# Performance work log

Hardware: AMD Instinct MI355X
Metric: run time of the kernel (lower is better)

The kernel has to match this reference:

```python
import jax, jax.numpy as jnp
import numpy as np

N_NODES = 50000
N_EDGES = 800000
IN_FEATS = 512
NUM_HEADS = 4
OUT_FEATS = 64
NEG_SLOPE = 0.2


def setup_inputs() -> dict:
    key = jax.random.key(0)
    k1, k2, k3, k4, k5, k6 = jax.random.split(key, 6)
    feat = jax.random.normal(k1, (N_NODES, IN_FEATS), dtype=jnp.float32)
    W = jax.random.normal(k2, (IN_FEATS, NUM_HEADS * OUT_FEATS), dtype=jnp.float32) * (1.0 / np.sqrt(IN_FEATS))
    attn_l = jax.random.normal(k3, (NUM_HEADS, OUT_FEATS), dtype=jnp.float32) * (1.0 / np.sqrt(OUT_FEATS))
    attn_r = jax.random.normal(k4, (NUM_HEADS, OUT_FEATS), dtype=jnp.float32) * (1.0 / np.sqrt(OUT_FEATS))
    src = jax.random.randint(k5, (N_EDGES,), 0, N_NODES, dtype=jnp.int32)
    dst = jax.random.randint(k6, (N_EDGES,), 0, N_NODES, dtype=jnp.int32)
    return {"feat": feat, "W": W, "attn_l": attn_l, "attn_r": attn_r, "src": src, "dst": dst}


def reference(feat, W, attn_l, attn_r, src, dst):
    N = feat.shape[0]
    H, D = attn_l.shape
    # node-wise projection: fc(feat).view(N, H, D)
    ft = (feat @ W).reshape(N, H, D)
    # per-node attention logits
    el = jnp.einsum('nhd,hd->nh', ft, attn_l)  # [N, H]
    er = jnp.einsum('nhd,hd->nh', ft, attn_r)  # [N, H]
    # edge-wise score: leaky_relu(el[u] + er[v])
    e = jax.nn.leaky_relu(el[src] + er[dst], negative_slope=NEG_SLOPE)  # [E, H]
    # segment softmax over incoming edges of each destination node
    e_max = jax.ops.segment_max(e, dst, num_segments=N)  # [N, H]
    e_max = jnp.where(jnp.isfinite(e_max), e_max, 0.0)
    exp_e = jnp.exp(e - e_max[dst])  # [E, H]
    denom = jax.ops.segment_sum(exp_e, dst, num_segments=N)  # [N, H]
    a = exp_e / denom[dst]  # [E, H]
    # weighted message aggregation: sum_u a(u,v) * ft[u]
    msg = ft[src] * a[:, :, None]  # [E, H, D]
    out = jax.ops.segment_sum(msg, dst, num_segments=N)  # [N, H, D]
    return out.reshape(N, H * D)
```

## Files before the change

kernel.cpp:

```cpp
#include <hip/hip_runtime.h>
#include <hip/hip_fp16.h>

#define N_NODES 50000
#define N_EDGES 800000
#define IN_F    512
#define NH      4
#define DH      64
#define HD      256
#define NEG     0.2f
#define MAXDEG  64

typedef __attribute__((ext_vector_type(8))) short bf16x8;
typedef __attribute__((ext_vector_type(4))) float f32x4;

__device__ __forceinline__ unsigned short f2bf(float x) {
    unsigned u = __float_as_uint(x);
    unsigned r = (u + 0x7FFFu + ((u >> 16) & 1u)) >> 16;
    return (unsigned short)r;
}
__device__ __forceinline__ float bf2f(unsigned short b) {
    return __uint_as_float((unsigned)b << 16);
}
__device__ __forceinline__ unsigned short f2h(float x) {
    __half h = __float2half_rn(x);
    return *(unsigned short*)&h;
}
__device__ __forceinline__ float h2f(unsigned short us) {
    __half h = *(__half*)&us;
    return __half2float(h);
}

#define NZB ((N_NODES + 255) / 256)
__global__ __launch_bounds__(256) void setup_kernel(const float* __restrict__ W,
                                                    unsigned short* __restrict__ WtbT,
                                                    int* __restrict__ counts) {
    int b = blockIdx.x;
    if (b < NZB) {
        int i = b * 256 + threadIdx.x;
        if (i < N_NODES) counts[i] = 0;
    } else {
        int i = (b - NZB) * 256 + threadIdx.x;
        if (i < IN_F * HD) {
            int k = i >> 8;
            int n = i & 255;
            int t  = k >> 6;
            int kk = k & 63;
            int g  = kk >> 3;
            int w8 = kk & 7;
            int p  = n * 8 + (g ^ (n & 7));
            WtbT[(size_t)t * 16384 + p * 8 + w8] = f2bf(W[i]);
        }
    }
}

#define LDPA 72
__global__ __launch_bounds__(256) void gemm_kernel(const float* __restrict__ A,
                                                   const unsigned short* __restrict__ WtbT,
                                                   const float* __restrict__ attn_l,
                                                   const float* __restrict__ attn_r,
                                                   unsigned short* __restrict__ Cb,
                                                   float* __restrict__ el,
                                                   float* __restrict__ er) {
    __shared__ short A_s[64][LDPA];
    __shared__ short B_s[2][256 * 64];

    const int tid  = threadIdx.x;
    const int lane = tid & 63;
    const int w    = tid >> 6;
    const int lm   = lane & 15;
    const int quad = lane >> 4;
    const int row0 = blockIdx.x * 64;

    const int srow = tid >> 3;
    const int sc8  = (tid & 7) * 8;

    f32x4 acc[4][4] = {};
    float4 pa[4];

#define STAGE_B(BUF, T)                                                         \
    {                                                                           \
        const char* gsrc = (const char*)WtbT + (size_t)(T) * 32768 + tid * 16;  \
        char* ldst = (char*)&B_s[BUF][0] + tid * 16;                            \
        _Pragma("unroll")                                                       \
        for (int r = 0; r < 8; r++)                                             \
            __builtin_amdgcn_global_load_lds(                                   \
                (const __attribute__((address_space(1))) unsigned int*)(gsrc + r * 4096), \
                (__attribute__((address_space(3))) unsigned int*)(ldst + r * 4096),       \
                16, 0, 0);                                                      \
    }

#define LOAD_A(KT)                                                             \
    {                                                                          \
        int g0 = row0 + srow;                                                  \
        if (g0 < N_NODES) {                                                    \
            const float* ap = A + (size_t)g0 * IN_F + (KT) + sc8;              \
            pa[0] = *(const float4*)ap; pa[1] = *(const float4*)(ap + 4);      \
        } else { pa[0] = pa[1] = make_float4(0.f, 0.f, 0.f, 0.f); }            \
        int g1 = row0 + 32 + srow;                                             \
        if (g1 < N_NODES) {                                                    \
            const float* ap = A + (size_t)g1 * IN_F + (KT) + sc8;              \
            pa[2] = *(const float4*)ap; pa[3] = *(const float4*)(ap + 4);      \
        } else { pa[2] = pa[3] = make_float4(0.f, 0.f, 0.f, 0.f); }            \
    }

    STAGE_B(0, 0);
    LOAD_A(0);

    int buf = 0;
    for (int t = 0; t < 8; t++) {
        {
            bf16x8 s;
            s[0] = (short)f2bf(pa[0].x); s[1] = (short)f2bf(pa[0].y);
            s[2] = (short)f2bf(pa[0].z); s[3] = (short)f2bf(pa[0].w);
            s[4] = (short)f2bf(pa[1].x); s[5] = (short)f2bf(pa[1].y);
            s[6] = (short)f2bf(pa[1].z); s[7] = (short)f2bf(pa[1].w);
            *(bf16x8*)(&A_s[srow][sc8]) = s;
            s[0] = (short)f2bf(pa[2].x); s[1] = (short)f2bf(pa[2].y);
            s[2] = (short)f2bf(pa[2].z); s[3] = (short)f2bf(pa[2].w);
            s[4] = (short)f2bf(pa[3].x); s[5] = (short)f2bf(pa[3].y);
            s[6] = (short)f2bf(pa[3].z); s[7] = (short)f2bf(pa[3].w);
            *(bf16x8*)(&A_s[32 + srow][sc8]) = s;
        }
        __syncthreads();

        if (t + 1 < 8) { STAGE_B(buf ^ 1, t + 1); LOAD_A((t + 1) * 64); }

#pragma unroll
        for (int kk = 0; kk < 64; kk += 32) {
            bf16x8 af[4], bfr[4];
#pragma unroll
            for (int i = 0; i < 4; i++)
                af[i] = *(const bf16x8*)(&A_s[i * 16 + lm][kk + quad * 8]);
#pragma unroll
            for (int j = 0; j < 4; j++) {
                int n  = w * 64 + j * 16 + lm;
                int g  = (kk >> 3) + quad;
                int gs = g ^ (lm & 7);
                bfr[j] = *(const bf16x8*)(&B_s[buf][(n * 8 + gs) * 8]);
            }
#pragma unroll
            for (int i = 0; i < 4; i++)
#pragma unroll
                for (int j = 0; j < 4; j++)
                    acc[i][j] = __builtin_amdgcn_mfma_f32_16x16x32_bf16(
                        af[i], bfr[j], acc[i][j], 0, 0, 0);
        }
        if (t < 7) __syncthreads();
        buf ^= 1;
    }
#undef LOAD_A
#undef STAGE_B

#pragma unroll
    for (int i = 0; i < 4; i++) {
#pragma unroll
        for (int j = 0; j < 4; j++) {
            int gcol = w * 64 + j * 16 + lm;
#pragma unroll
            for (int r = 0; r < 4; r++) {
                int grow = row0 + i * 16 + quad * 4 + r;
                if (grow < N_NODES)
                    Cb[(size_t)grow * HD + gcol] = f2bf(acc[i][j][r]);
            }
        }
    }

    {
        float al[4], ar[4];
#pragma unroll
        for (int j = 0; j < 4; j++) {
            al[j] = attn_l[w * DH + j * 16 + lm];
            ar[j] = attn_r[w * DH + j * 16 + lm];
        }
#pragma unroll
        for (int i = 0; i < 4; i++) {
#pragma unroll
            for (int r = 0; r < 4; r++) {
                float sl = 0.f, sr = 0.f;
#pragma unroll
                for (int j = 0; j < 4; j++) {
                    sl += acc[i][j][r] * al[j];
                    sr += acc[i][j][r] * ar[j];
                }
#pragma unroll
                for (int off = 8; off > 0; off >>= 1) {
                    sl += __shfl_xor(sl, off);
                    sr += __shfl_xor(sr, off);
                }
                if (lm == 0) {
                    int grow = row0 + i * 16 + quad * 4 + r;
                    if (grow < N_NODES) {
                        el[(size_t)grow * NH + w] = sl;
                        er[(size_t)grow * NH + w] = sr;
                    }
                }
            }
        }
    }
}

__device__ __forceinline__ float lrelu_exp(float x) {
    float y = fmaxf(x, NEG * x);
    return fminf(__expf(y), 60000.f);
}

__global__ __launch_bounds__(256) void place_kernel(const int* __restrict__ src,
                                                    const int* __restrict__ dst,
                                                    const float* __restrict__ el,
                                                    const float* __restrict__ er,
                                                    int* __restrict__ counts,
                                                    int4* __restrict__ recs) {
    int e = blockIdx.x * blockDim.x + threadIdx.x;
    if (e >= N_EDGES) return;
    int u = src[e], v = dst[e];
    float4 l = *(const float4*)(el + (size_t)u * NH);
    float4 r = *(const float4*)(er + (size_t)v * NH);
    float w0 = lrelu_exp(l.x + r.x);
    float w1 = lrelu_exp(l.y + r.y);
    float w2 = lrelu_exp(l.z + r.z);
    float w3 = lrelu_exp(l.w + r.w);
    int4 rec;
    rec.x = u;
    rec.y = (int)(((unsigned)f2h(w1) << 16) | (unsigned)f2h(w0));
    rec.z = (int)(((unsigned)f2h(w3) << 16) | (unsigned)f2h(w2));
    rec.w = 0;
    int j = atomicAdd(&counts[v], 1);
    if (j < MAXDEG) recs[(size_t)v * MAXDEG + j] = rec;
}

__global__ __launch_bounds__(256) void agg_kernel(const unsigned short* __restrict__ ftb,
                                                  const int4* __restrict__ recs,
                                                  const int* __restrict__ counts,
                                                  float* __restrict__ out) {
    int wv   = (blockIdx.x * blockDim.x + threadIdx.x) >> 6;
    int lane = threadIdx.x & 63;
    if (wv >= N_NODES) return;

    int deg = counts[wv];
    deg = (deg > MAXDEG) ? MAXDEG : deg;
    const int h    = lane >> 4;
    const int sh   = (h & 1) * 16;
    const int wsel = 1 + (h >> 1);
    const size_t foff = (size_t)lane * 4;
    const unsigned* rp = (const unsigned*)(recs + (size_t)wv * MAXDEG);

    float4 acc = make_float4(0.f, 0.f, 0.f, 0.f);
    float dsum = 0.f;

    const int n8 = deg >> 3;
    for (int b = 0; b < n8; b++) {
        const unsigned* q = rp + b * 32;
        unsigned u0 = q[0],  p0 = q[0  + wsel];
        unsigned u1 = q[4],  p1 = q[4  + wsel];
        unsigned u2 = q[8],  p2 = q[8  + wsel];
        unsigned u3 = q[12], p3 = q[12 + wsel];
        unsigned u4 = q[16], p4 = q[16 + wsel];
        unsigned u5 = q[20], p5 = q[20 + wsel];
        unsigned u6 = q[24], p6 = q[24 + wsel];
        unsigned u7 = q[28], p7 = q[28 + wsel];
        ushort4 f0 = *(const ushort4*)(ftb + (size_t)u0 * HD + foff);
        ushort4 f1 = *(const ushort4*)(ftb + (size_t)u1 * HD + foff);
        ushort4 f2 = *(const ushort4*)(ftb + (size_t)u2 * HD + foff);
        ushort4 f3 = *(const ushort4*)(ftb + (size_t)u3 * HD + foff);
        ushort4 f4 = *(const ushort4*)(ftb + (size_t)u4 * HD + foff);
        ushort4 f5 = *(const ushort4*)(ftb + (size_t)u5 * HD + foff);
        ushort4 f6 = *(const ushort4*)(ftb + (size_t)u6 * HD + foff);
        ushort4 f7 = *(const ushort4*)(ftb + (size_t)u7 * HD + foff);
        float w0 = h2f((unsigned short)((p0 >> sh) & 0xFFFFu));
        float w1 = h2f((unsigned short)((p1 >> sh) & 0xFFFFu));
        float w2 = h2f((unsigned short)((p2 >> sh) & 0xFFFFu));
        float w3 = h2f((unsigned short)((p3 >> sh) & 0xFFFFu));
        float w4 = h2f((unsigned short)((p4 >> sh) & 0xFFFFu));
        float w5 = h2f((unsigned short)((p5 >> sh) & 0xFFFFu));
        float w6 = h2f((unsigned short)((p6 >> sh) & 0xFFFFu));
        float w7 = h2f((unsigned short)((p7 >> sh) & 0xFFFFu));
        acc.x += w0 * bf2f(f0.x) + w1 * bf2f(f1.x) + w2 * bf2f(f2.x) + w3 * bf2f(f3.x)
               + w4 * bf2f(f4.x) + w5 * bf2f(f5.x) + w6 * bf2f(f6.x) + w7 * bf2f(f7.x);
        acc.y += w0 * bf2f(f0.y) + w1 * bf2f(f1.y) + w2 * bf2f(f2.y) + w3 * bf2f(f3.y)
               + w4 * bf2f(f4.y) + w5 * bf2f(f5.y) + w6 * bf2f(f6.y) + w7 * bf2f(f7.y);
        acc.z += w0 * bf2f(f0.z) + w1 * bf2f(f1.z) + w2 * bf2f(f2.z) + w3 * bf2f(f3.z)
               + w4 * bf2f(f4.z) + w5 * bf2f(f5.z) + w6 * bf2f(f6.z) + w7 * bf2f(f7.z);
        acc.w += w0 * bf2f(f0.w) + w1 * bf2f(f1.w) + w2 * bf2f(f2.w) + w3 * bf2f(f3.w)
               + w4 * bf2f(f4.w) + w5 * bf2f(f5.w) + w6 * bf2f(f6.w) + w7 * bf2f(f7.w);
        dsum += ((w0 + w1) + (w2 + w3)) + ((w4 + w5) + (w6 + w7));
    }
    {
        const int p0i = n8 * 8;
        const int rem = deg - p0i;
        if (rem > 0) {
            const unsigned* q = rp + p0i * 4;
            unsigned u0 = q[0];
            unsigned u1 = (1 < rem) ? q[4]  : u0;
            unsigned u2 = (2 < rem) ? q[8]  : u0;
            unsigned u3 = (3 < rem) ? q[12] : u0;
            unsigned u4 = (4 < rem) ? q[16] : u0;
            unsigned u5 = (5 < rem) ? q[20] : u0;
            unsigned u6 = (6 < rem) ? q[24] : u0;
            unsigned p0 = q[0 + wsel];
            unsigned p1 = (1 < rem) ? q[4  + wsel] : 0u;
            unsigned p2 = (2 < rem) ? q[8  + wsel] : 0u;
            unsigned p3 = (3 < rem) ? q[12 + wsel] : 0u;
            unsigned p4 = (4 < rem) ? q[16 + wsel] : 0u;
            unsigned p5 = (5 < rem) ? q[20 + wsel] : 0u;
            unsigned p6 = (6 < rem) ? q[24 + wsel] : 0u;
            ushort4 f0 = *(const ushort4*)(ftb + (size_t)u0 * HD + foff);
            ushort4 f1 = *(const ushort4*)(ftb + (size_t)u1 * HD + foff);
            ushort4 f2 = *(const ushort4*)(ftb + (size_t)u2 * HD + foff);
            ushort4 f3 = *(const ushort4*)(ftb + (size_t)u3 * HD + foff);
            ushort4 f4 = *(const ushort4*)(ftb + (size_t)u4 * HD + foff);
            ushort4 f5 = *(const ushort4*)(ftb + (size_t)u5 * HD + foff);
            ushort4 f6 = *(const ushort4*)(ftb + (size_t)u6 * HD + foff);
            float w0 = h2f((unsigned short)((p0 >> sh) & 0xFFFFu));
            float w1 = h2f((unsigned short)((p1 >> sh) & 0xFFFFu));
            float w2 = h2f((unsigned short)((p2 >> sh) & 0xFFFFu));
            float w3 = h2f((unsigned short)((p3 >> sh) & 0xFFFFu));
            float w4 = h2f((unsigned short)((p4 >> sh) & 0xFFFFu));
            float w5 = h2f((unsigned short)((p5 >> sh) & 0xFFFFu));
            float w6 = h2f((unsigned short)((p6 >> sh) & 0xFFFFu));
            acc.x += w0 * bf2f(f0.x) + w1 * bf2f(f1.x) + w2 * bf2f(f2.x) + w3 * bf2f(f3.x)
                   + w4 * bf2f(f4.x) + w5 * bf2f(f5.x) + w6 * bf2f(f6.x);
            acc.y += w0 * bf2f(f0.y) + w1 * bf2f(f1.y) + w2 * bf2f(f2.y) + w3 * bf2f(f3.y)
                   + w4 * bf2f(f4.y) + w5 * bf2f(f5.y) + w6 * bf2f(f6.y);
            acc.z += w0 * bf2f(f0.z) + w1 * bf2f(f1.z) + w2 * bf2f(f2.z) + w3 * bf2f(f3.z)
                   + w4 * bf2f(f4.z) + w5 * bf2f(f5.z) + w6 * bf2f(f6.z);
            acc.w += w0 * bf2f(f0.w) + w1 * bf2f(f1.w) + w2 * bf2f(f2.w) + w3 * bf2f(f3.w)
                   + w4 * bf2f(f4.w) + w5 * bf2f(f5.w) + w6 * bf2f(f6.w);
            dsum += ((w0 + w1) + (w2 + w3)) + ((w4 + w5) + w6);
        }
    }

    float inv = (dsum > 0.f) ? (1.f / dsum) : 0.f;
    acc.x *= inv; acc.y *= inv; acc.z *= inv; acc.w *= inv;
    *(float4*)(out + (size_t)wv * HD + foff) = acc;
}

extern "C" void kernel_launch(void* const* d_in, const int* in_sizes, int n_in,
                              void* d_out, int out_size, void* d_ws, size_t ws_size,
                              hipStream_t stream) {
    const float* feat   = (const float*)d_in[0];
    const float* W      = (const float*)d_in[1];
    const float* attn_l = (const float*)d_in[2];
    const float* attn_r = (const float*)d_in[3];
    const int*   src    = (const int*)d_in[4];
    const int*   dst    = (const int*)d_in[5];
    float* out = (float*)d_out;

    char* p = (char*)d_ws;
    auto alloc = [&](size_t bytes) -> char* {
        char* r = p;
        p += (bytes + 255) & ~(size_t)255;
        return r;
    };
    unsigned short* ftb    = (unsigned short*)alloc((size_t)N_NODES * HD * 2);
    unsigned short* WtbT   = (unsigned short*)alloc((size_t)IN_F * HD * 2);
    float*          el     = (float*)alloc((size_t)N_NODES * NH * 4);
    float*          er     = (float*)alloc((size_t)N_NODES * NH * 4);
    int4*           recs   = (int4*)alloc((size_t)N_NODES * MAXDEG * 16);
    int*            counts = (int*)alloc((size_t)N_NODES * 4);

    setup_kernel<<<NZB + (IN_F * HD + 255) / 256, 256, 0, stream>>>(W, WtbT, counts);
    gemm_kernel<<<(N_NODES + 63) / 64, 256, 0, stream>>>(feat, WtbT, attn_l, attn_r,
                                                         ftb, el, er);
    place_kernel<<<(N_EDGES + 255) / 256, 256, 0, stream>>>(src, dst, el, er,
                                                            counts, recs);
    agg_kernel<<<(N_NODES + 3) / 4, 256, 0, stream>>>(ftb, recs, counts, out);
}
```

Measured before the change: 301.7 us.

## Load W fragments directly from global into registers; double-buffer A in LDS

The weight layout is changed to a k-group-major order so that each lane can read its B fragments for the MFMA straight from global memory (via L2) into registers. This removes the 64 KB B staging in LDS. The A tile is now double-buffered in LDS, which needs only one barrier per k-step instead of two, and row clamping replaces the branchy bounds checks. The cost is that every block issues redundant global reads of W, and global load latency now sits on the MFMA path. In exchange, LDS use drops sharply, which may allow higher occupancy.

```diff
diff --git a/kernel.cpp b/kernel.cpp
--- a/kernel.cpp
+++ b/kernel.cpp
@@ -47,8 +47,7 @@
             int kk = k & 63;
             int g  = kk >> 3;
             int w8 = kk & 7;
-            int p  = n * 8 + (g ^ (n & 7));
-            WtbT[(size_t)t * 16384 + p * 8 + w8] = f2bf(W[i]);
+            WtbT[(size_t)t * 16384 + g * 2048 + n * 8 + w8] = f2bf(W[i]);
         }
     }
 }
@@ -61,8 +60,7 @@
                                                    unsigned short* __restrict__ Cb,
                                                    float* __restrict__ el,
                                                    float* __restrict__ er) {
-    __shared__ short A_s[64][LDPA];
-    __shared__ short B_s[2][256 * 64];
+    __shared__ short A_s[2][64][LDPA];
 
     const int tid  = threadIdx.x;
     const int lane = tid & 63;
@@ -77,79 +75,79 @@
     f32x4 acc[4][4] = {};
     float4 pa[4];
 
-#define STAGE_B(BUF, T)                                                         \
-    {                                                                           \
-        const char* gsrc = (const char*)WtbT + (size_t)(T) * 32768 + tid * 16;  \
-        char* ldst = (char*)&B_s[BUF][0] + tid * 16;                            \
-        _Pragma("unroll")                                                       \
-        for (int r = 0; r < 8; r++)                                             \
-            __builtin_amdgcn_global_load_lds(                                   \
-                (const __attribute__((address_space(1))) unsigned int*)(gsrc + r * 4096), \
-                (__attribute__((address_space(3))) unsigned int*)(ldst + r * 4096),       \
-                16, 0, 0);                                                      \
-    }
-
 #define LOAD_A(KT)                                                             \
     {                                                                          \
-        int g0 = row0 + srow;                                                  \
-        if (g0 < N_NODES) {                                                    \
-            const float* ap = A + (size_t)g0 * IN_F + (KT) + sc8;              \
-            pa[0] = *(const float4*)ap; pa[1] = *(const float4*)(ap + 4);      \
-        } else { pa[0] = pa[1] = make_float4(0.f, 0.f, 0.f, 0.f); }            \
-        int g1 = row0 + 32 + srow;                                             \
-        if (g1 < N_NODES) {                                                    \
-            const float* ap = A + (size_t)g1 * IN_F + (KT) + sc8;              \
-            pa[2] = *(const float4*)ap; pa[3] = *(const float4*)(ap + 4);      \
-        } else { pa[2] = pa[3] = make_float4(0.f, 0.f, 0.f, 0.f); }            \
-    }
-
-    STAGE_B(0, 0);
+        int g0 = row0 + srow; g0 = (g0 < N_NODES) ? g0 : (N_NODES - 1);        \
+        const float* ap0 = A + (size_t)g0 * IN_F + (KT) + sc8;                 \
+        pa[0] = *(const float4*)ap0; pa[1] = *(const float4*)(ap0 + 4);        \
+        int g1 = row0 + 32 + srow; g1 = (g1 < N_NODES) ? g1 : (N_NODES - 1);   \
+        const float* ap1 = A + (size_t)g1 * IN_F + (KT) + sc8;                 \
+        pa[2] = *(const float4*)ap1; pa[3] = *(const float4*)(ap1 + 4);        \
+    }
+
+#define CVT_STORE(BUF)                                                         \
+    {                                                                          \
+        bf16x8 s;                                                              \
+        s[0] = (short)f2bf(pa[0].x); s[1] = (short)f2bf(pa[0].y);              \
+        s[2] = (short)f2bf(pa[0].z); s[3] = (short)f2bf(pa[0].w);              \
+        s[4] = (short)f2bf(pa[1].x); s[5] = (short)f2bf(pa[1].y);              \
+        s[6] = (short)f2bf(pa[1].z); s[7] = (short)f2bf(pa[1].w);              \
+        *(bf16x8*)(&A_s[BUF][srow][sc8]) = s;                                  \
+        s[0] = (short)f2bf(pa[2].x); s[1] = (short)f2bf(pa[2].y);              \
+        s[2] = (short)f2bf(pa[2].z); s[3] = (short)f2bf(pa[2].w);              \
+        s[4] = (short)f2bf(pa[3].x); s[5] = (short)f2bf(pa[3].y);              \
+        s[6] = (short)f2bf(pa[3].z); s[7] = (short)f2bf(pa[3].w);              \
+        *(bf16x8*)(&A_s[BUF][32 + srow][sc8]) = s;                             \
+    }
+
     LOAD_A(0);
-
-    int buf = 0;
+    CVT_STORE(0);
+    __syncthreads();
+
     for (int t = 0; t < 8; t++) {
+        const int cur = t & 1;
+        const unsigned short* bq =
+            WtbT + (size_t)t * 16384 + ((quad << 8) + w * 64 + lm) * 8;
+        bf16x8 bfr0[4], bfr1[4];
+#pragma unroll
+        for (int j = 0; j < 4; j++) bfr0[j] = *(const bf16x8*)(bq + j * 128);
+#pragma unroll
+        for (int j = 0; j < 4; j++) bfr1[j] = *(const bf16x8*)(bq + 8192 + j * 128);
+
+        if (t < 7) LOAD_A((t + 1) * 64);
+
         {
-            bf16x8 s;
-            s[0] = (short)f2bf(pa[0].x); s[1] = (short)f2bf(pa[0].y);
-            s[2] = (short)f2bf(pa[0].z); s[3] = (short)f2bf(pa[0].w);
-            s[4] = (short)f2bf(pa[1].x); s[5] = (short)f2bf(pa[1].y);
-            s[6] = (short)f2bf(pa[1].z); s[7] = (short)f2bf(pa[1].w);
-            *(bf16x8*)(&A_s[srow][sc8]) = s;
-            s[0] = (short)f2bf(pa[2].x); s[1] = (short)f2bf(pa[2].y);
-            s[2] = (short)f2bf(pa[2].z); s[3] = (short)f2bf(pa[2].w);
-            s[4] = (short)f2bf(pa[3].x); s[5] = (short)f2bf(pa[3].y);
-            s[6] = (short)f2bf(pa[3].z); s[7] = (short)f2bf(pa[3].w);
-            *(bf16x8*)(&A_s[32 + srow][sc8]) = s;
-        }
-        __syncthreads();
-
-        if (t + 1 < 8) { STAGE_B(buf ^ 1, t + 1); LOAD_A((t + 1) * 64); }
-
-#pragma unroll
-        for (int kk = 0; kk < 64; kk += 32) {
-            bf16x8 af[4], bfr[4];
+            bf16x8 af[4];
 #pragma unroll
             for (int i = 0; i < 4; i++)
-                af[i] = *(const bf16x8*)(&A_s[i * 16 + lm][kk + quad * 8]);
-#pragma unroll
-            for (int j = 0; j < 4; j++) {
-                int n  = w * 64 + j * 16 + lm;
-                int g  = (kk >> 3) + quad;
-                int gs = g ^ (lm & 7);
-                bfr[j] = *(const bf16x8*)(&B_s[buf][(n * 8 + gs) * 8]);
-            }
+                af[i] = *(const bf16x8*)(&A_s[cur][i * 16 + lm][quad * 8]);
 #pragma unroll
             for (int i = 0; i < 4; i++)
 #pragma unroll
                 for (int j = 0; j < 4; j++)
                     acc[i][j] = __builtin_amdgcn_mfma_f32_16x16x32_bf16(
-                        af[i], bfr[j], acc[i][j], 0, 0, 0);
-        }
-        if (t < 7) __syncthreads();
-        buf ^= 1;
+                        af[i], bfr0[j], acc[i][j], 0, 0, 0);
+        }
+        {
+            bf16x8 af[4];
+#pragma unroll
+            for (int i = 0; i < 4; i++)
+                af[i] = *(const bf16x8*)(&A_s[cur][i * 16 + lm][32 + quad * 8]);
+#pragma unroll
+            for (int i = 0; i < 4; i++)
+#pragma unroll
+                for (int j = 0; j < 4; j++)
+                    acc[i][j] = __builtin_amdgcn_mfma_f32_16x16x32_bf16(
+                        af[i], bfr1[j], acc[i][j], 0, 0, 0);
+        }
+
+        if (t < 7) {
+            CVT_STORE(cur ^ 1);
+            __syncthreads();
+        }
     }
 #undef LOAD_A
-#undef STAGE_B
+#undef CVT_STORE
 
 #pragma unroll
     for (int i = 0; i < 4; i++) {
```

Result: no change. 305.5 us (+1.2%).

## Pre-convert features to swizzled bf16 tiles and load A via direct LDS

Applied to the files above, without the earlier changes.

Adds a conversion kernel that writes feat as bf16 in a per-row-block tiled, XOR-swizzled layout. The GEMM then streams A and B tiles with global_load_lds instead of converting fp32 in registers, and drops double buffering. This is meant to remove per-thread conversion work and register staging from the GEMM. The cost is an extra full pass over the input with a bf16 intermediate buffer, and load latency is no longer overlapped with MFMA work.

```diff
diff --git a/kernel.cpp b/kernel.cpp
--- a/kernel.cpp
+++ b/kernel.cpp
@@ -9,6 +9,8 @@
 #define HD      256
 #define NEG     0.2f
 #define MAXDEG  64
+#define NRB     ((N_NODES + 63) / 64)
+#define NROWS_P (NRB * 64)
 
 typedef __attribute__((ext_vector_type(8))) short bf16x8;
 typedef __attribute__((ext_vector_type(4))) float f32x4;
@@ -47,96 +49,88 @@
             int kk = k & 63;
             int g  = kk >> 3;
             int w8 = kk & 7;
-            int p  = n * 8 + (g ^ (n & 7));
-            WtbT[(size_t)t * 16384 + p * 8 + w8] = f2bf(W[i]);
-        }
-    }
-}
-
-#define LDPA 72
-__global__ __launch_bounds__(256) void gemm_kernel(const float* __restrict__ A,
+            WtbT[(size_t)t * 16384 + (n * 8 + (g ^ (n & 7))) * 8 + w8] = f2bf(W[i]);
+        }
+    }
+}
+
+__global__ __launch_bounds__(256) void cvt_kernel(const float* __restrict__ feat,
+                                                  unsigned short* __restrict__ fbf) {
+    int gid = blockIdx.x * 256 + threadIdx.x;
+    if (gid >= NROWS_P * 64) return;
+    int n = gid >> 6;
+    int l = gid & 63;
+    int t = l >> 3;
+    int g = l & 7;
+    int rb = n >> 6;
+    int r  = n & 63;
+    bf16x8 s = {};
+    if (n < N_NODES) {
+        const float* fp = feat + (size_t)n * IN_F + l * 8;
+        float4 a = *(const float4*)fp;
+        float4 b = *(const float4*)(fp + 4);
+        s[0] = (short)f2bf(a.x); s[1] = (short)f2bf(a.y);
+        s[2] = (short)f2bf(a.z); s[3] = (short)f2bf(a.w);
+        s[4] = (short)f2bf(b.x); s[5] = (short)f2bf(b.y);
+        s[6] = (short)f2bf(b.z); s[7] = (short)f2bf(b.w);
+    }
+    *(bf16x8*)(fbf + ((size_t)rb * 8 + t) * 4096 + (r * 8 + (g ^ (r & 7))) * 8) = s;
+}
+
+__global__ __launch_bounds__(256) void gemm_kernel(const unsigned short* __restrict__ fbf,
                                                    const unsigned short* __restrict__ WtbT,
                                                    const float* __restrict__ attn_l,
                                                    const float* __restrict__ attn_r,
                                                    unsigned short* __restrict__ Cb,
                                                    float* __restrict__ el,
                                                    float* __restrict__ er) {
-    __shared__ short A_s[64][LDPA];
-    __shared__ short B_s[2][256 * 64];
+    __shared__ short A_s[4096];
+    __shared__ short B_s[16384];
 
     const int tid  = threadIdx.x;
     const int lane = tid & 63;
     const int w    = tid >> 6;
     const int lm   = lane & 15;
     const int quad = lane >> 4;
-    const int row0 = blockIdx.x * 64;
-
-    const int srow = tid >> 3;
-    const int sc8  = (tid & 7) * 8;
+    const int rb   = blockIdx.x;
+    const int row0 = rb * 64;
 
     f32x4 acc[4][4] = {};
-    float4 pa[4];
-
-#define STAGE_B(BUF, T)                                                         \
-    {                                                                           \
-        const char* gsrc = (const char*)WtbT + (size_t)(T) * 32768 + tid * 16;  \
-        char* ldst = (char*)&B_s[BUF][0] + tid * 16;                            \
-        _Pragma("unroll")                                                       \
-        for (int r = 0; r < 8; r++)                                             \
-            __builtin_amdgcn_global_load_lds(                                   \
-                (const __attribute__((address_space(1))) unsigned int*)(gsrc + r * 4096), \
-                (__attribute__((address_space(3))) unsigned int*)(ldst + r * 4096),       \
-                16, 0, 0);                                                      \
-    }
-
-#define LOAD_A(KT)                                                             \
-    {                                                                          \
-        int g0 = row0 + srow;                                                  \
-        if (g0 < N_NODES) {                                                    \
-            const float* ap = A + (size_t)g0 * IN_F + (KT) + sc8;              \
-            pa[0] = *(const float4*)ap; pa[1] = *(const float4*)(ap + 4);      \
-        } else { pa[0] = pa[1] = make_float4(0.f, 0.f, 0.f, 0.f); }            \
-        int g1 = row0 + 32 + srow;                                             \
-        if (g1 < N_NODES) {                                                    \
-            const float* ap = A + (size_t)g1 * IN_F + (KT) + sc8;              \
-            pa[2] = *(const float4*)ap; pa[3] = *(const float4*)(ap + 4);      \
-        } else { pa[2] = pa[3] = make_float4(0.f, 0.f, 0.f, 0.f); }            \
-    }
-
-    STAGE_B(0, 0);
-    LOAD_A(0);
-
-    int buf = 0;
+
     for (int t = 0; t < 8; t++) {
         {
-            bf16x8 s;
-            s[0] = (short)f2bf(pa[0].x); s[1] = (short)f2bf(pa[0].y);
-            s[2] = (short)f2bf(pa[0].z); s[3] = (short)f2bf(pa[0].w);
-            s[4] = (short)f2bf(pa[1].x); s[5] = (short)f2bf(pa[1].y);
-            s[6] = (short)f2bf(pa[1].z); s[7] = (short)f2bf(pa[1].w);
-            *(bf16x8*)(&A_s[srow][sc8]) = s;
-            s[0] = (short)f2bf(pa[2].x); s[1] = (short)f2bf(pa[2].y);
-            s[2] = (short)f2bf(pa[2].z); s[3] = (short)f2bf(pa[2].w);
-            s[4] = (short)f2bf(pa[3].x); s[5] = (short)f2bf(pa[3].y);
-            s[6] = (short)f2bf(pa[3].z); s[7] = (short)f2bf(pa[3].w);
-            *(bf16x8*)(&A_s[32 + srow][sc8]) = s;
+            const char* ga = (const char*)(fbf + ((size_t)rb * 8 + t) * 4096) + tid * 16;
+            char* la = (char*)A_s + tid * 16;
+#pragma unroll
+            for (int s = 0; s < 2; s++)
+                __builtin_amdgcn_global_load_lds(
+                    (const __attribute__((address_space(1))) unsigned int*)(ga + s * 4096),
+                    (__attribute__((address_space(3))) unsigned int*)(la + s * 4096),
+                    16, 0, 0);
+            const char* gb = (const char*)(WtbT + (size_t)t * 16384) + tid * 16;
+            char* lb = (char*)B_s + tid * 16;
+#pragma unroll
+            for (int s = 0; s < 8; s++)
+                __builtin_amdgcn_global_load_lds(
+                    (const __attribute__((address_space(1))) unsigned int*)(gb + s * 4096),
+                    (__attribute__((address_space(3))) unsigned int*)(lb + s * 4096),
+                    16, 0, 0);
         }
         __syncthreads();
 
-        if (t + 1 < 8) { STAGE_B(buf ^ 1, t + 1); LOAD_A((t + 1) * 64); }
-
-#pragma unroll
-        for (int kk = 0; kk < 64; kk += 32) {
+#pragma unroll
+        for (int kk2 = 0; kk2 < 2; kk2++) {
+            const int g = kk2 * 4 + quad;
             bf16x8 af[4], bfr[4];
 #pragma unroll
-            for (int i = 0; i < 4; i++)
-                af[i] = *(const bf16x8*)(&A_s[i * 16 + lm][kk + quad * 8]);
+            for (int i = 0; i < 4; i++) {
+                int r = i * 16 + lm;
+                af[i] = *(const bf16x8*)(&A_s[(r * 8 + (g ^ (r & 7))) * 8]);
+            }
 #pragma unroll
             for (int j = 0; j < 4; j++) {
-                int n  = w * 64 + j * 16 + lm;
-                int g  = (kk >> 3) + quad;
-                int gs = g ^ (lm & 7);
-                bfr[j] = *(const bf16x8*)(&B_s[buf][(n * 8 + gs) * 8]);
+                int n = w * 64 + j * 16 + lm;
+                bfr[j] = *(const bf16x8*)(&B_s[(n * 8 + (g ^ (n & 7))) * 8]);
             }
 #pragma unroll
             for (int i = 0; i < 4; i++)
@@ -146,10 +140,7 @@
                         af[i], bfr[j], acc[i][j], 0, 0, 0);
         }
         if (t < 7) __syncthreads();
-        buf ^= 1;
-    }
-#undef LOAD_A
-#undef STAGE_B
+    }
 
 #pragma unroll
     for (int i = 0; i < 4; i++) {
@@ -351,6 +342,7 @@
         p += (bytes + 255) & ~(size_t)255;
         return r;
     };
+    unsigned short* fbf    = (unsigned short*)alloc((size_t)NROWS_P * IN_F * 2);
     unsigned short* ftb    = (unsigned short*)alloc((size_t)N_NODES * HD * 2);
     unsigned short* WtbT   = (unsigned short*)alloc((size_t)IN_F * HD * 2);
     float*          el     = (float*)alloc((size_t)N_NODES * NH * 4);
@@ -359,8 +351,8 @@
     int*            counts = (int*)alloc((size_t)N_NODES * 4);
 
     setup_kernel<<<NZB + (IN_F * HD + 255) / 256, 256, 0, stream>>>(W, WtbT, counts);
-    gemm_kernel<<<(N_NODES + 63) / 64, 256, 0, stream>>>(feat, WtbT, attn_l, attn_r,
-                                                         ftb, el, er);
+    cvt_kernel<<<(NROWS_P * 64 + 255) / 256, 256, 0, stream>>>(feat, fbf);
+    gemm_kernel<<<NRB, 256, 0, stream>>>(fbf, WtbT, attn_l, attn_r, ftb, el, er);
     place_kernel<<<(N_EDGES + 255) / 256, 256, 0, stream>>>(src, dst, el, er,
                                                             counts, recs);
     agg_kernel<<<(N_NODES + 3) / 4, 256, 0, stream>>>(ftb, recs, counts, out);
```

Result: slower. 321.1 us (+6.4%).
